# Kernel tuning notes

Hardware: AMD Instinct MI355X
Metric: run time of the kernel (lower is better)

The kernel has to match this reference:

```python
import jax, jax.numpy as jnp
import numpy as np

T, B, NOBS = 128, 4096, 32
LOG_2PI = float(np.log(2.0 * np.pi))


def setup_inputs() -> dict:
    key = jax.random.key(0)
    k1, k2, k3 = jax.random.split(key, 3)
    Y = jax.random.normal(k1, (T, B, NOBS), dtype=jnp.float32)
    Yhat = jax.random.normal(k2, (T, B, NOBS), dtype=jnp.float32)
    raw_sn = jnp.zeros((NOBS,), dtype=jnp.float32)  # learned noise param (init zeros)
    kl = jax.random.uniform(k3, (), dtype=jnp.float32)  # external sgp.kl() scalar
    N = 10000
    return {"Y": Y, "Yhat": Yhat, "raw_sn": raw_sn, "kl": kl, "N": N}


def reference(Y, Yhat, raw_sn, kl, N):
    # cov = diag(softplus(raw_sn)); MVN(loc=Y, cov).log_prob(Yhat)
    var = jax.nn.softplus(raw_sn)  # [nobs] per-dim variance
    diff = Yhat - Y  # [T, B, nobs]
    nobs = raw_sn.shape[0]
    # diagonal-cov MVN log_prob: -0.5*(maha + logdet + nobs*log(2pi))
    maha = jnp.sum(diff * diff / var, axis=-1)  # [T, B]
    logdet = jnp.sum(jnp.log(var))
    logp = -0.5 * (maha + logdet + nobs * LOG_2PI)  # [T, B]
    lhood = jnp.mean(jnp.sum(logp, axis=0)) * N  # scalar
    return -lhood + kl
```

## Files before the change

### kernel.cpp

```cpp
#include <hip/hip_runtime.h>
#include <math.h>

#define T_DIM 128
#define B_DIM 4096
#define NOBS  32
#define LOG_2PI 1.8378770664093453f

constexpr int BLOCKS  = 2048;
constexpr int THREADS = 256;
constexpr int TOTAL_ELEMS = T_DIM * B_DIM * NOBS;
constexpr int TOTAL4      = TOTAL_ELEMS / 4;

__device__ __forceinline__ float softplus_f(float x) {
    return fmaxf(x, 0.0f) + log1pf(expf(-fabsf(x)));
}

__global__ __launch_bounds__(THREADS) void elbo_partial_kernel(
    const float* __restrict__ Y,
    const float* __restrict__ Yhat,
    const float* __restrict__ raw_sn,
    float* __restrict__ partial)
{
    __shared__ float sh_iv[NOBS];
    const int tid = threadIdx.x;
    if (tid < NOBS) {
        sh_iv[tid] = 1.0f / softplus_f(raw_sn[tid]);
    }
    __syncthreads();

    const int gtid = blockIdx.x * THREADS + tid;
    const int d0 = (gtid * 4) & (NOBS - 1);
    const float iv0 = sh_iv[d0 + 0];
    const float iv1 = sh_iv[d0 + 1];
    const float iv2 = sh_iv[d0 + 2];
    const float iv3 = sh_iv[d0 + 3];

    const float4* __restrict__ Y4 = (const float4*)Y;
    const float4* __restrict__ H4 = (const float4*)Yhat;

    float acc = 0.0f;
    const int stride = BLOCKS * THREADS;
    for (int i = gtid; i < TOTAL4; i += stride) {
        float4 y = Y4[i];
        float4 h = H4[i];
        float dx = h.x - y.x;
        float dy = h.y - y.y;
        float dz = h.z - y.z;
        float dw = h.w - y.w;
        acc = fmaf(dx * dx, iv0, acc);
        acc = fmaf(dy * dy, iv1, acc);
        acc = fmaf(dz * dz, iv2, acc);
        acc = fmaf(dw * dw, iv3, acc);
    }

    #pragma unroll
    for (int off = 32; off > 0; off >>= 1)
        acc += __shfl_down(acc, off, 64);

    __shared__ float sh_sum[THREADS / 64];
    const int wave = tid >> 6;
    const int lane = tid & 63;
    if (lane == 0) sh_sum[wave] = acc;
    __syncthreads();
    if (tid == 0) {
        float s = 0.0f;
        #pragma unroll
        for (int w = 0; w < THREADS / 64; ++w) s += sh_sum[w];
        partial[blockIdx.x] = s;
    }
}

__global__ __launch_bounds__(256) void elbo_final_kernel(
    const float* __restrict__ partial,
    const float* __restrict__ raw_sn,
    const float* __restrict__ kl,
    const int*   __restrict__ Nptr,
    float* __restrict__ out)
{
    const int tid = threadIdx.x;
    float acc = 0.0f;
    for (int i = tid; i < BLOCKS; i += 256) acc += partial[i];

    #pragma unroll
    for (int off = 32; off > 0; off >>= 1)
        acc += __shfl_down(acc, off, 64);

    __shared__ float sh[4];
    if ((tid & 63) == 0) sh[tid >> 6] = acc;
    __syncthreads();

    if (tid == 0) {
        float S = sh[0] + sh[1] + sh[2] + sh[3];
        float logdet = 0.0f;
        #pragma unroll
        for (int d = 0; d < NOBS; ++d) {
            logdet += logf(softplus_f(raw_sn[d]));
        }
        float inner = S / (float)B_DIM + (float)T_DIM * (logdet + (float)NOBS * LOG_2PI);
        out[0] = 0.5f * (float)(*Nptr) * inner + kl[0];
    }
}

extern "C" void kernel_launch(void* const* d_in, const int* in_sizes, int n_in,
                              void* d_out, int out_size, void* d_ws, size_t ws_size,
                              hipStream_t stream) {
    const float* Y      = (const float*)d_in[0];
    const float* Yhat   = (const float*)d_in[1];
    const float* raw_sn = (const float*)d_in[2];
    const float* kl     = (const float*)d_in[3];
    const int*   N      = (const int*)d_in[4];
    float* partial = (float*)d_ws;
    float* out     = (float*)d_out;

    elbo_partial_kernel<<<BLOCKS, THREADS, 0, stream>>>(Y, Yhat, raw_sn, partial);
    elbo_final_kernel<<<1, 256, 0, stream>>>(partial, raw_sn, kl, N, out);
}
```

Measured before the change: 163.7 us.

## Stage Y through LDS via global_load_lds DMA and issue all loads upfront

Replaces the grid-stride loop with a fully unrolled fixed count of 8 iterations per thread. All Y tiles are fetched by asynchronous global-to-LDS DMA while all Yhat vectors are loaded into registers before a single barrier. Independent partial accumulators replace the single serial one. The aim is more memory requests in flight and less load latency on a bandwidth-bound reduction. The cost is 32KB of LDS per block, which may limit occupancy, and reliance on the compiler to wait on the DMA before the barrier.

```diff
diff --git a/kernel.cpp b/kernel.cpp
--- a/kernel.cpp
+++ b/kernel.cpp
@@ -8,11 +8,23 @@
 
 constexpr int BLOCKS  = 2048;
 constexpr int THREADS = 256;
+constexpr int WAVES   = THREADS / 64;
 constexpr int TOTAL_ELEMS = T_DIM * B_DIM * NOBS;
 constexpr int TOTAL4      = TOTAL_ELEMS / 4;
+constexpr int ITERS   = TOTAL4 / (BLOCKS * THREADS);
+
+typedef float f32x4 __attribute__((ext_vector_type(4)));
+
+#define GLOBAL_AS __attribute__((address_space(1)))
+#define LDS_AS    __attribute__((address_space(3)))
 
 __device__ __forceinline__ float softplus_f(float x) {
     return fmaxf(x, 0.0f) + log1pf(expf(-fabsf(x)));
+}
+
+__device__ __forceinline__ void dma_lds_16(const void* g, void* l) {
+    __builtin_amdgcn_global_load_lds((const GLOBAL_AS void*)g,
+                                     (LDS_AS void*)l, 16, 0,  2);
 }
 
 __global__ __launch_bounds__(THREADS) void elbo_partial_kernel(
@@ -21,51 +33,60 @@
     const float* __restrict__ raw_sn,
     float* __restrict__ partial)
 {
+    __shared__ f32x4 sh_y[ITERS * THREADS];
     __shared__ float sh_iv[NOBS];
-    const int tid = threadIdx.x;
-    if (tid < NOBS) {
-        sh_iv[tid] = 1.0f / softplus_f(raw_sn[tid]);
+    __shared__ float sh_sum[WAVES];
+
+    const int tid  = threadIdx.x;
+    const int wave = tid >> 6;
+    const int lane = tid & 63;
+
+    if (tid < NOBS) sh_iv[tid] = 1.0f / softplus_f(raw_sn[tid]);
+
+    const int gtid = blockIdx.x * THREADS + tid;
+    const int d0 = (gtid * 4) & (NOBS - 1);
+
+    const f32x4* __restrict__ Y4 = (const f32x4*)Y;
+    const f32x4* __restrict__ H4 = (const f32x4*)Yhat;
+    constexpr int stride = BLOCKS * THREADS;
+
+    f32x4 h[ITERS];
+    #pragma unroll
+    for (int m = 0; m < ITERS; ++m) {
+        dma_lds_16(&Y4[gtid + m * stride], &sh_y[(m * WAVES + wave) * 64]);
+        h[m] = H4[gtid + m * stride];
     }
     __syncthreads();
 
-    const int gtid = blockIdx.x * THREADS + tid;
-    const int d0 = (gtid * 4) & (NOBS - 1);
     const float iv0 = sh_iv[d0 + 0];
     const float iv1 = sh_iv[d0 + 1];
     const float iv2 = sh_iv[d0 + 2];
     const float iv3 = sh_iv[d0 + 3];
 
-    const float4* __restrict__ Y4 = (const float4*)Y;
-    const float4* __restrict__ H4 = (const float4*)Yhat;
+    float a0 = 0.0f, a1 = 0.0f, a2 = 0.0f, a3 = 0.0f;
+    #pragma unroll
+    for (int m = 0; m < ITERS; ++m) {
+        f32x4 y  = sh_y[(m * WAVES + wave) * 64 + lane];
+        f32x4 hh = h[m];
+        float d;
+        d = hh.x - y.x; a0 = fmaf(d * d, iv0, a0);
+        d = hh.y - y.y; a1 = fmaf(d * d, iv1, a1);
+        d = hh.z - y.z; a2 = fmaf(d * d, iv2, a2);
+        d = hh.w - y.w; a3 = fmaf(d * d, iv3, a3);
+    }
 
-    float acc = 0.0f;
-    const int stride = BLOCKS * THREADS;
-    for (int i = gtid; i < TOTAL4; i += stride) {
-        float4 y = Y4[i];
-        float4 h = H4[i];
-        float dx = h.x - y.x;
-        float dy = h.y - y.y;
-        float dz = h.z - y.z;
-        float dw = h.w - y.w;
-        acc = fmaf(dx * dx, iv0, acc);
-        acc = fmaf(dy * dy, iv1, acc);
-        acc = fmaf(dz * dz, iv2, acc);
-        acc = fmaf(dw * dw, iv3, acc);
-    }
+    float acc = (a0 + a1) + (a2 + a3);
 
     #pragma unroll
     for (int off = 32; off > 0; off >>= 1)
         acc += __shfl_down(acc, off, 64);
 
-    __shared__ float sh_sum[THREADS / 64];
-    const int wave = tid >> 6;
-    const int lane = tid & 63;
     if (lane == 0) sh_sum[wave] = acc;
     __syncthreads();
     if (tid == 0) {
         float s = 0.0f;
         #pragma unroll
-        for (int w = 0; w < THREADS / 64; ++w) s += sh_sum[w];
+        for (int w = 0; w < WAVES; ++w) s += sh_sum[w];
         partial[blockIdx.x] = s;
     }
 }
```

Measured after the change: 148.7 us. 9.2% less time.
